# Kernel tuning notes

Hardware: AMD Instinct MI355X
Metric: run time of the kernel (lower is better)

Reference implementation:

```python
import jax, jax.numpy as jnp
import numpy as np

N_NODES = 50000
N_EDGES = 800000
IN_CH, HID_CH, OUT_CH = 128, 128, 40


def setup_inputs() -> dict:
    key = jax.random.key(0)
    k1, k2, k3, k4 = jax.random.split(key, 4)
    x = jax.random.normal(k1, (N_NODES, IN_CH), dtype=jnp.float32)
    edge_index = jax.random.randint(k2, (2, N_EDGES), 0, N_NODES, dtype=jnp.int64)
    # Glorot-ish init for linear weights
    W1 = jax.random.normal(k3, (IN_CH, HID_CH), dtype=jnp.float32) / np.sqrt(IN_CH)
    b1 = jnp.zeros((HID_CH,), dtype=jnp.float32)
    W2 = jax.random.normal(k4, (HID_CH, OUT_CH), dtype=jnp.float32) / np.sqrt(HID_CH)
    b2 = jnp.zeros((OUT_CH,), dtype=jnp.float32)
    return {"x": x, "edge_index": edge_index, "W1": W1, "b1": b1, "W2": W2, "b2": b2}


def _gcn_conv(x, src, dst, W, b):
    # GCNConv(normalize=False): dense transform then sparse aggregation (scatter-add)
    h = x @ W                                   # [N, C_out]
    out = jax.ops.segment_sum(h[src], dst, num_segments=N_NODES)  # sum_{j->i} h[j]
    return out + b


def reference(x, edge_index, W1, b1, W2, b2):
    src, dst = edge_index[0], edge_index[1]
    h = _gcn_conv(x, src, dst, W1, b1)
    h = jax.nn.relu(h)
    # dropout is identity in eval mode
    h = _gcn_conv(h, src, dst, W2, b2)
    return jax.nn.log_softmax(h, axis=-1)
```

## Files before the change

kernel.cpp:

```cpp
#include <hip/hip_runtime.h>

#define NN 50000
#define NE 800000
#define NBKT 196
#define NB_BIN 128
#define EPB (NE / NB_BIN)
#define MATN (NBKT * NB_BIN)

using short8 = __attribute__((ext_vector_type(8))) short;
using f32x4  = __attribute__((ext_vector_type(4))) float;
union U4S8 { uint4 u; short8 v; };

__device__ __forceinline__ float lof(unsigned v) { return __uint_as_float(v << 16); }
__device__ __forceinline__ float hif(unsigned v) { return __uint_as_float(v & 0xffff0000u); }
__device__ __forceinline__ unsigned bf16rne(float f) {
    unsigned u = __float_as_uint(f);
    return (u + 0x7fffu + ((u >> 16) & 1u)) >> 16;
}
__device__ __forceinline__ unsigned pack2(float a, float b) {
    return bf16rne(a) | (bf16rne(b) << 16);
}
__device__ __forceinline__ unsigned fp8pack4(float a0, float a1, float a2, float a3) {
    int w = __builtin_amdgcn_cvt_pk_fp8_f32(a0, a1, 0, false);
    w = __builtin_amdgcn_cvt_pk_fp8_f32(a2, a3, w, true);
    return (unsigned)w;
}

__global__ __launch_bounds__(256) void binhist_k(const int* __restrict__ dst,
                                                 int* __restrict__ mat,
                                                 const float* __restrict__ W1,
                                                 const float* __restrict__ W2,
                                                 unsigned* __restrict__ W1T,
                                                 unsigned* __restrict__ W2T) {
    __shared__ int hist[NBKT];
    const int tid = threadIdx.x;
    for (int i = tid; i < NBKT; i += 256) hist[i] = 0;

    const int g = blockIdx.x * 256 + tid;
    if (g < 8192) {
        const int n = g >> 6, k2 = (g & 63) * 2;
        W1T[g] = pack2(W1[k2 * 128 + n], W1[(k2 + 1) * 128 + n]);
    } else if (g < 8192 + 3072) {
        const int u = g - 8192;
        const int n = u >> 6;
        const int q0 = (u & 63) * 2, q1 = q0 + 1;
        const int c0 = (q0 & 7) * 16 + (q0 >> 3);
        const int c1 = (q1 & 7) * 16 + (q1 >> 3);
        W2T[u] = (n < 40) ? pack2(W2[c0 * 40 + n], W2[c1 * 40 + n]) : 0u;
    }
    __syncthreads();

    const int base = blockIdx.x * EPB;
    for (int e = base + tid; e < base + EPB; e += 256)
        atomicAdd(&hist[dst[e] >> 8], 1);
    __syncthreads();
    for (int i = tid; i < NBKT; i += 256)
        mat[i * NB_BIN + blockIdx.x] = hist[i];
}

__global__ __launch_bounds__(256) void binscatter_k(const int* __restrict__ src,
                                                    const int* __restrict__ dst,
                                                    const int* __restrict__ mat,
                                                    unsigned* __restrict__ binned,
                                                    int* __restrict__ bucketoff) {
    __shared__ int lds[MATN];
    __shared__ int tsum[256];
    const int tid = threadIdx.x;
    for (int i = tid; i < MATN; i += 256) lds[i] = mat[i];
    __syncthreads();
    const int b0 = tid * (MATN / 256);
    int s = 0;
#pragma unroll 7
    for (int i = 0; i < MATN / 256; ++i) s += lds[b0 + i];
    tsum[tid] = s;
    __syncthreads();
#pragma unroll
    for (int off = 1; off < 256; off <<= 1) {
        int u = (tid >= off) ? tsum[tid - off] : 0;
        __syncthreads();
        tsum[tid] += u;
        __syncthreads();
    }
    int run = tsum[tid] - s;
#pragma unroll 7
    for (int i = 0; i < MATN / 256; ++i) {
        const int v = lds[b0 + i]; lds[b0 + i] = run; run += v;
    }
    __syncthreads();

    if (blockIdx.x == 0) {
        for (int i = tid; i < NBKT; i += 256) bucketoff[i] = lds[i * NB_BIN];
        if (tid == 0) bucketoff[NBKT] = NE;
        __syncthreads();
    }

    const int base = blockIdx.x * EPB;
    for (int e = base + tid; e < base + EPB; e += 256) {
        const int d = dst[e];
        const int p = atomicAdd(&lds[(d >> 8) * NB_BIN + blockIdx.x], 1);
        binned[p] = ((unsigned)(d & 255) << 16) | (unsigned)src[e];
    }
}

__global__ __launch_bounds__(256) void bucketcsr_k(const unsigned* __restrict__ binned,
                                                   const int* __restrict__ bucketoff,
                                                   int* __restrict__ rowoff,
                                                   unsigned short* __restrict__ eid) {
    __shared__ int cnt[256];
    __shared__ int off[256];
    const int b = blockIdx.x;
    const int tid = threadIdx.x;
    const int beg = bucketoff[b];
    const int end = bucketoff[b + 1];
    cnt[tid] = 0;
    __syncthreads();
    for (int i = beg + tid; i < end; i += 256)
        atomicAdd(&cnt[(binned[i] >> 16) & 255u], 1);
    __syncthreads();
    const int v = cnt[tid];
    off[tid] = v;
    __syncthreads();
#pragma unroll
    for (int o = 1; o < 256; o <<= 1) {
        int u = (tid >= o) ? off[tid - o] : 0;
        __syncthreads();
        off[tid] += u;
        __syncthreads();
    }
    const int excl = off[tid] - v;
    const int node = b * 256 + tid;
    if (node <= NN) rowoff[node] = beg + excl;
    cnt[tid] = excl;
    __syncthreads();
    for (int i = beg + tid; i < end; i += 256) {
        const unsigned e = binned[i];
        const int p = atomicAdd(&cnt[(e >> 16) & 255u], 1);
        eid[beg + p] = (unsigned short)(e & 0xffffu);
    }
}

__global__ __launch_bounds__(256) void gemm1_k(const float* __restrict__ x,
                                               const unsigned* __restrict__ W1T,
                                               uint2* __restrict__ H1) {
    const int lane = threadIdx.x & 63;
    const int cl = lane & 15;
    const int kh = lane >> 4;
    const int gw = (blockIdx.x * 256 + threadIdx.x) >> 6;

    short8 Bf[8][4];
#pragma unroll
    for (int c = 0; c < 8; ++c)
#pragma unroll
        for (int kc = 0; kc < 4; ++kc) {
            U4S8 tb;
            tb.u = *(const uint4*)(W1T + ((c * 16 + cl) * 128 + kc * 32 + kh * 8) / 2);
            Bf[c][kc] = tb.v;
        }

    for (int mt = gw; mt < 3125; mt += 2048) {
        const int r0 = mt * 16;
        const float* ap = x + (long)(r0 + cl) * 128 + kh * 8;
        f32x4 acc[8];
#pragma unroll
        for (int c = 0; c < 8; ++c) acc[c] = (f32x4){0.f, 0.f, 0.f, 0.f};
#pragma unroll
        for (int kc = 0; kc < 4; ++kc) {
            const float4 p0 = *(const float4*)(ap + kc * 32);
            const float4 p1 = *(const float4*)(ap + kc * 32 + 4);
            U4S8 af;
            af.u.x = pack2(p0.x, p0.y);
            af.u.y = pack2(p0.z, p0.w);
            af.u.z = pack2(p1.x, p1.y);
            af.u.w = pack2(p1.z, p1.w);
#pragma unroll
            for (int c = 0; c < 8; ++c)
                acc[c] = __builtin_amdgcn_mfma_f32_16x16x32_bf16(af.v, Bf[c][kc], acc[c], 0, 0, 0);
        }
#pragma unroll
        for (int j = 0; j < 4; ++j) {
            uint2 o;
            o.x = fp8pack4(acc[0][j], acc[1][j], acc[2][j], acc[3][j]);
            o.y = fp8pack4(acc[4][j], acc[5][j], acc[6][j], acc[7][j]);
            H1[(long)(r0 + kh * 4 + j) * 16 + cl] = o;
        }
    }
}

__global__ __launch_bounds__(256) void gather1_k(const uint2* __restrict__ H1,
                                                 const int* __restrict__ rowoff,
                                                 const unsigned short* __restrict__ eid,
                                                 const float* __restrict__ b1,
                                                 uint4* __restrict__ h) {
    const int n = blockIdx.x * 4 + (threadIdx.x >> 6);
    const int lane = threadIdx.x & 63;
    const int g = lane >> 4;
    const int cl = lane & 15;
    const int beg = rowoff[n], end = rowoff[n + 1];
    float a[8] = {0.f, 0.f, 0.f, 0.f, 0.f, 0.f, 0.f, 0.f};

#define ACC8(v)                                                              \
    {                                                                        \
        auto t0 = __builtin_amdgcn_cvt_pk_f32_fp8((int)(v).x, false);        \
        auto t1 = __builtin_amdgcn_cvt_pk_f32_fp8((int)(v).x, true);         \
        auto t2 = __builtin_amdgcn_cvt_pk_f32_fp8((int)(v).y, false);        \
        auto t3 = __builtin_amdgcn_cvt_pk_f32_fp8((int)(v).y, true);         \
        a[0] += t0[0]; a[1] += t0[1]; a[2] += t1[0]; a[3] += t1[1];          \
        a[4] += t2[0]; a[5] += t2[1]; a[6] += t3[0]; a[7] += t3[1];          \
    }

    int k = beg;
    for (; k + 7 < end; k += 8) {
        const int sA = eid[k + g];
        const int sB = eid[k + 4 + g];
        const uint2 vA = H1[sA * 16 + cl];
        const uint2 vB = H1[sB * 16 + cl];
        ACC8(vA);
        ACC8(vB);
    }
    for (; k + 3 < end; k += 4) {
        const uint2 v = H1[eid[k + g] * 16 + cl];
        ACC8(v);
    }
    if (k + g < end) {
        const uint2 v = H1[eid[k + g] * 16 + cl];
        ACC8(v);
    }
#undef ACC8

#pragma unroll
    for (int i = 0; i < 8; ++i) {
        a[i] += __shfl_xor(a[i], 16, 64);
        a[i] += __shfl_xor(a[i], 32, 64);
    }
    if (lane < 16) {
        float r[8];
#pragma unroll
        for (int i = 0; i < 8; ++i) r[i] = fmaxf(a[i] + b1[i * 16 + cl], 0.f);
        uint4 o;
        o.x = pack2(r[0], r[1]);
        o.y = pack2(r[2], r[3]);
        o.z = pack2(r[4], r[5]);
        o.w = pack2(r[6], r[7]);
        h[n * 16 + cl] = o;
    }
}

__global__ __launch_bounds__(256) void gemm2_k(const unsigned* __restrict__ h,
                                               const unsigned* __restrict__ W2T,
                                               unsigned short* __restrict__ H2) {
    const int lane = threadIdx.x & 63;
    const int cl = lane & 15;
    const int kh = lane >> 4;
    const int gw = (blockIdx.x * 256 + threadIdx.x) >> 6;

    short8 Bf[3][4];
#pragma unroll
    for (int c = 0; c < 3; ++c)
#pragma unroll
        for (int kc = 0; kc < 4; ++kc) {
            U4S8 tb;
            tb.u = *(const uint4*)(W2T + ((c * 16 + cl) * 128 + kc * 32 + kh * 8) / 2);
            Bf[c][kc] = tb.v;
        }

    for (int mt = gw; mt < 3125; mt += 2048) {
        const int r0 = mt * 16;
        const unsigned* ap = h + (long)(r0 + cl) * 64 + kh * 4;
        f32x4 acc[3];
#pragma unroll
        for (int c = 0; c < 3; ++c) acc[c] = (f32x4){0.f, 0.f, 0.f, 0.f};
#pragma unroll
        for (int kc = 0; kc < 4; ++kc) {
            U4S8 af;
            af.u = *(const uint4*)(ap + kc * 16);
#pragma unroll
            for (int c = 0; c < 3; ++c)
                acc[c] = __builtin_amdgcn_mfma_f32_16x16x32_bf16(af.v, Bf[c][kc], acc[c], 0, 0, 0);
        }
        unsigned short* hp = H2 + (long)(r0 + kh * 4) * 64;
#pragma unroll
        for (int c = 0; c < 3; ++c) {
            const int col = c * 16 + cl;
            if (col < 40) {
#pragma unroll
                for (int j = 0; j < 4; ++j)
                    hp[j * 64 + col] = (unsigned short)bf16rne(acc[c][j]);
            }
        }
    }
}

__global__ __launch_bounds__(256) void gather2_k(const unsigned* __restrict__ H2,
                                                 const int* __restrict__ rowoff,
                                                 const unsigned short* __restrict__ eid,
                                                 const float* __restrict__ b2,
                                                 float* __restrict__ out) {
    const int n = blockIdx.x * 4 + (threadIdx.x >> 6);
    const int lane = threadIdx.x & 63;
    const int g = lane / 20;
    const int c2 = lane - g * 20;
    const int beg = rowoff[n], end = rowoff[n + 1];
    float ax = 0.f, ay = 0.f;
    if (g < 3) {
        int k = beg + g;
        for (; k + 3 < end; k += 6) {
            const int s0 = eid[k], s1 = eid[k + 3];
            const unsigned v0 = H2[s0 * 32 + c2];
            const unsigned v1 = H2[s1 * 32 + c2];
            ax += lof(v0) + lof(v1);
            ay += hif(v0) + hif(v1);
        }
        if (k < end) {
            const unsigned v = H2[eid[k] * 32 + c2];
            ax += lof(v); ay += hif(v);
        }
    }
    ax += __shfl(ax, lane + 20, 64) + __shfl(ax, lane + 40, 64);
    ay += __shfl(ay, lane + 20, 64) + __shfl(ay, lane + 40, 64);

    const bool act = (lane < 20);
    float2 b = {0.f, 0.f};
    if (act) b = ((const float2*)b2)[lane];
    const float vx = ax + b.x, vy = ay + b.y;
    float m = act ? fmaxf(vx, vy) : -INFINITY;
#pragma unroll
    for (int off = 32; off; off >>= 1) m = fmaxf(m, __shfl_xor(m, off, 64));
    float e = act ? (expf(vx - m) + expf(vy - m)) : 0.f;
#pragma unroll
    for (int off = 32; off; off >>= 1) e += __shfl_xor(e, off, 64);
    const float ls = logf(e);
    if (act) {
        float2 o = {vx - m - ls, vy - m - ls};
        ((float2*)out)[n * 20 + lane] = o;
    }
}

extern "C" void kernel_launch(void* const* d_in, const int* in_sizes, int n_in,
                              void* d_out, int out_size, void* d_ws, size_t ws_size,
                              hipStream_t stream) {
    const float* x  = (const float*)d_in[0];
    const int*   ei = (const int*)d_in[1];
    const float* W1 = (const float*)d_in[2];
    const float* b1 = (const float*)d_in[3];
    const float* W2 = (const float*)d_in[4];
    const float* b2 = (const float*)d_in[5];
    const int* src = ei;
    const int* dst = ei + NE;

    unsigned* H1   = (unsigned*)d_ws;
    unsigned* h    = H1 + (size_t)NN * 32;
    unsigned* H2   = h + (size_t)NN * 64;
    unsigned* W1T  = H2 + (size_t)NN * 32;
    unsigned* W2T  = W1T + 8192;
    int* mat       = (int*)(W2T + 3072);
    int* bucketoff = mat + MATN;
    int* rowoff    = bucketoff + NBKT + 1;
    unsigned short* eid = (unsigned short*)(rowoff + NN + 1);
    unsigned* binned = h;
    float* out     = (float*)d_out;

    binhist_k<<<NB_BIN, 256, 0, stream>>>(dst, mat, W1, W2, W1T, W2T);
    binscatter_k<<<NB_BIN, 256, 0, stream>>>(src, dst, mat, binned, bucketoff);
    bucketcsr_k<<<NBKT, 256, 0, stream>>>(binned, bucketoff, rowoff, eid);
    gemm1_k<<<512, 256, 0, stream>>>(x, W1T, (uint2*)H1);
    gather1_k<<<12500, 256, 0, stream>>>((const uint2*)H1, rowoff, eid, b1, (uint4*)h);
    gemm2_k<<<512, 256, 0, stream>>>(h, W2T, (unsigned short*)H2);
    gather2_k<<<12500, 256, 0, stream>>>(H2, rowoff, eid, b2, out);
}
```

Baseline: 121.9 us.

## Fuse CSR build with GEMM1, widen gather loads, shrink binning and GEMM grids

Merges the bucket-CSR kernel and the first GEMM into one launch so the two independent stages run concurrently across blocks, removing a kernel boundary. The gathers now use wider per-lane loads (uint4 fp8 rows for layer 1, uint2 bf16 for layer 2) with more edges in flight per wavefront. The binning block count and GEMM grid sizes are halved. Together these aim to cut launch overhead and raise memory-level parallelism in the gathers, at the cost of fewer lanes per row and more shuffle reduction steps.

```diff
diff --git a/kernel.cpp b/kernel.cpp
--- a/kernel.cpp
+++ b/kernel.cpp
@@ -3,9 +3,10 @@
 #define NN 50000
 #define NE 800000
 #define NBKT 196
-#define NB_BIN 128
+#define NB_BIN 64
 #define EPB (NE / NB_BIN)
 #define MATN (NBKT * NB_BIN)
+#define MCH (MATN / 256)
 
 using short8 = __attribute__((ext_vector_type(8))) short;
 using f32x4  = __attribute__((ext_vector_type(4))) float;
@@ -68,10 +69,10 @@
     const int tid = threadIdx.x;
     for (int i = tid; i < MATN; i += 256) lds[i] = mat[i];
     __syncthreads();
-    const int b0 = tid * (MATN / 256);
+    const int b0 = tid * MCH;
     int s = 0;
 #pragma unroll 7
-    for (int i = 0; i < MATN / 256; ++i) s += lds[b0 + i];
+    for (int i = 0; i < MCH; ++i) s += lds[b0 + i];
     tsum[tid] = s;
     __syncthreads();
 #pragma unroll
@@ -83,7 +84,7 @@
     }
     int run = tsum[tid] - s;
 #pragma unroll 7
-    for (int i = 0; i < MATN / 256; ++i) {
+    for (int i = 0; i < MCH; ++i) {
         const int v = lds[b0 + i]; lds[b0 + i] = run; run += v;
     }
     __syncthreads();
@@ -102,50 +103,51 @@
     }
 }
 
-__global__ __launch_bounds__(256) void bucketcsr_k(const unsigned* __restrict__ binned,
-                                                   const int* __restrict__ bucketoff,
-                                                   int* __restrict__ rowoff,
-                                                   unsigned short* __restrict__ eid) {
+__global__ __launch_bounds__(256) void csrgemm1_k(const unsigned* __restrict__ binned,
+                                                  const int* __restrict__ bucketoff,
+                                                  int* __restrict__ rowoff,
+                                                  unsigned short* __restrict__ eid,
+                                                  const float* __restrict__ x,
+                                                  const unsigned* __restrict__ W1T,
+                                                  uint2* __restrict__ H1) {
     __shared__ int cnt[256];
     __shared__ int off[256];
-    const int b = blockIdx.x;
     const int tid = threadIdx.x;
-    const int beg = bucketoff[b];
-    const int end = bucketoff[b + 1];
-    cnt[tid] = 0;
-    __syncthreads();
-    for (int i = beg + tid; i < end; i += 256)
-        atomicAdd(&cnt[(binned[i] >> 16) & 255u], 1);
-    __syncthreads();
-    const int v = cnt[tid];
-    off[tid] = v;
-    __syncthreads();
-#pragma unroll
-    for (int o = 1; o < 256; o <<= 1) {
-        int u = (tid >= o) ? off[tid - o] : 0;
-        __syncthreads();
-        off[tid] += u;
-        __syncthreads();
-    }
-    const int excl = off[tid] - v;
-    const int node = b * 256 + tid;
-    if (node <= NN) rowoff[node] = beg + excl;
-    cnt[tid] = excl;
-    __syncthreads();
-    for (int i = beg + tid; i < end; i += 256) {
-        const unsigned e = binned[i];
-        const int p = atomicAdd(&cnt[(e >> 16) & 255u], 1);
-        eid[beg + p] = (unsigned short)(e & 0xffffu);
-    }
-}
-
-__global__ __launch_bounds__(256) void gemm1_k(const float* __restrict__ x,
-                                               const unsigned* __restrict__ W1T,
-                                               uint2* __restrict__ H1) {
-    const int lane = threadIdx.x & 63;
+    if (blockIdx.x < NBKT) {
+        const int b = blockIdx.x;
+        const int beg = bucketoff[b];
+        const int end = bucketoff[b + 1];
+        cnt[tid] = 0;
+        __syncthreads();
+        for (int i = beg + tid; i < end; i += 256)
+            atomicAdd(&cnt[(binned[i] >> 16) & 255u], 1);
+        __syncthreads();
+        const int v = cnt[tid];
+        off[tid] = v;
+        __syncthreads();
+#pragma unroll
+        for (int o = 1; o < 256; o <<= 1) {
+            int u = (tid >= o) ? off[tid - o] : 0;
+            __syncthreads();
+            off[tid] += u;
+            __syncthreads();
+        }
+        const int excl = off[tid] - v;
+        const int node = b * 256 + tid;
+        if (node <= NN) rowoff[node] = beg + excl;
+        cnt[tid] = excl;
+        __syncthreads();
+        for (int i = beg + tid; i < end; i += 256) {
+            const unsigned e = binned[i];
+            const int p = atomicAdd(&cnt[(e >> 16) & 255u], 1);
+            eid[beg + p] = (unsigned short)(e & 0xffffu);
+        }
+        return;
+    }
+    const int lane = tid & 63;
     const int cl = lane & 15;
     const int kh = lane >> 4;
-    const int gw = (blockIdx.x * 256 + threadIdx.x) >> 6;
+    const int gw = ((blockIdx.x - NBKT) * 256 + tid) >> 6;
 
     short8 Bf[8][4];
 #pragma unroll
@@ -157,7 +159,7 @@
             Bf[c][kc] = tb.v;
         }
 
-    for (int mt = gw; mt < 3125; mt += 2048) {
+    for (int mt = gw; mt < 3125; mt += 1024) {
         const int r0 = mt * 16;
         const float* ap = x + (long)(r0 + cl) * 128 + kh * 8;
         f32x4 acc[8];
@@ -186,62 +188,71 @@
     }
 }
 
-__global__ __launch_bounds__(256) void gather1_k(const uint2* __restrict__ H1,
+__global__ __launch_bounds__(256) void gather1_k(const uint4* __restrict__ H1,
                                                  const int* __restrict__ rowoff,
                                                  const unsigned short* __restrict__ eid,
                                                  const float* __restrict__ b1,
                                                  uint4* __restrict__ h) {
     const int n = blockIdx.x * 4 + (threadIdx.x >> 6);
     const int lane = threadIdx.x & 63;
-    const int g = lane >> 4;
-    const int cl = lane & 15;
+    const int g = lane >> 3;
+    const int cl = lane & 7;
     const int beg = rowoff[n], end = rowoff[n + 1];
-    float a[8] = {0.f, 0.f, 0.f, 0.f, 0.f, 0.f, 0.f, 0.f};
-
-#define ACC8(v)                                                              \
+    float a[16];
+#pragma unroll
+    for (int i = 0; i < 16; ++i) a[i] = 0.f;
+
+#define ACC16(v)                                                             \
     {                                                                        \
         auto t0 = __builtin_amdgcn_cvt_pk_f32_fp8((int)(v).x, false);        \
         auto t1 = __builtin_amdgcn_cvt_pk_f32_fp8((int)(v).x, true);         \
         auto t2 = __builtin_amdgcn_cvt_pk_f32_fp8((int)(v).y, false);        \
         auto t3 = __builtin_amdgcn_cvt_pk_f32_fp8((int)(v).y, true);         \
-        a[0] += t0[0]; a[1] += t0[1]; a[2] += t1[0]; a[3] += t1[1];          \
-        a[4] += t2[0]; a[5] += t2[1]; a[6] += t3[0]; a[7] += t3[1];          \
+        auto t4 = __builtin_amdgcn_cvt_pk_f32_fp8((int)(v).z, false);        \
+        auto t5 = __builtin_amdgcn_cvt_pk_f32_fp8((int)(v).z, true);         \
+        auto t6 = __builtin_amdgcn_cvt_pk_f32_fp8((int)(v).w, false);        \
+        auto t7 = __builtin_amdgcn_cvt_pk_f32_fp8((int)(v).w, true);         \
+        a[0] += t0[0];  a[1] += t0[1];  a[2] += t1[0];  a[3] += t1[1];       \
+        a[4] += t2[0];  a[5] += t2[1];  a[6] += t3[0];  a[7] += t3[1];       \
+        a[8] += t4[0];  a[9] += t4[1];  a[10] += t5[0]; a[11] += t5[1];      \
+        a[12] += t6[0]; a[13] += t6[1]; a[14] += t7[0]; a[15] += t7[1];      \
     }
 
     int k = beg;
+    for (; k + 15 < end; k += 16) {
+        const uint4 vA = H1[eid[k + g] * 8 + cl];
+        const uint4 vB = H1[eid[k + 8 + g] * 8 + cl];
+        ACC16(vA);
+        ACC16(vB);
+    }
     for (; k + 7 < end; k += 8) {
-        const int sA = eid[k + g];
-        const int sB = eid[k + 4 + g];
-        const uint2 vA = H1[sA * 16 + cl];
-        const uint2 vB = H1[sB * 16 + cl];
-        ACC8(vA);
-        ACC8(vB);
-    }
-    for (; k + 3 < end; k += 4) {
-        const uint2 v = H1[eid[k + g] * 16 + cl];
-        ACC8(v);
+        const uint4 v = H1[eid[k + g] * 8 + cl];
+        ACC16(v);
     }
     if (k + g < end) {
-        const uint2 v = H1[eid[k + g] * 16 + cl];
-        ACC8(v);
-    }
-#undef ACC8
-
-#pragma unroll
-    for (int i = 0; i < 8; ++i) {
+        const uint4 v = H1[eid[k + g] * 8 + cl];
+        ACC16(v);
+    }
+#undef ACC16
+
+#pragma unroll
+    for (int i = 0; i < 16; ++i) {
+        a[i] += __shfl_xor(a[i], 8, 64);
         a[i] += __shfl_xor(a[i], 16, 64);
         a[i] += __shfl_xor(a[i], 32, 64);
     }
-    if (lane < 16) {
-        float r[8];
-#pragma unroll
-        for (int i = 0; i < 8; ++i) r[i] = fmaxf(a[i] + b1[i * 16 + cl], 0.f);
-        uint4 o;
-        o.x = pack2(r[0], r[1]);
-        o.y = pack2(r[2], r[3]);
-        o.z = pack2(r[4], r[5]);
-        o.w = pack2(r[6], r[7]);
-        h[n * 16 + cl] = o;
+    if (lane < 8) {
+        float r[16];
+#pragma unroll
+        for (int i = 0; i < 16; ++i)
+            r[i] = fmaxf(a[i] + b1[(i & 7) * 16 + cl * 2 + (i >> 3)], 0.f);
+        uint4 o1, o2;
+        o1.x = pack2(r[0], r[1]);  o1.y = pack2(r[2], r[3]);
+        o1.z = pack2(r[4], r[5]);  o1.w = pack2(r[6], r[7]);
+        o2.x = pack2(r[8], r[9]);  o2.y = pack2(r[10], r[11]);
+        o2.z = pack2(r[12], r[13]); o2.w = pack2(r[14], r[15]);
+        h[n * 16 + cl * 2] = o1;
+        h[n * 16 + cl * 2 + 1] = o2;
     }
 }
 
@@ -263,7 +274,7 @@
             Bf[c][kc] = tb.v;
         }
 
-    for (int mt = gw; mt < 3125; mt += 2048) {
+    for (int mt = gw; mt < 3125; mt += 1024) {
         const int r0 = mt * 16;
         const unsigned* ap = h + (long)(r0 + cl) * 64 + kh * 4;
         f32x4 acc[3];
@@ -290,48 +301,54 @@
     }
 }
 
-__global__ __launch_bounds__(256) void gather2_k(const unsigned* __restrict__ H2,
+__global__ __launch_bounds__(256) void gather2_k(const uint2* __restrict__ H2,
                                                  const int* __restrict__ rowoff,
                                                  const unsigned short* __restrict__ eid,
                                                  const float* __restrict__ b2,
                                                  float* __restrict__ out) {
     const int n = blockIdx.x * 4 + (threadIdx.x >> 6);
     const int lane = threadIdx.x & 63;
-    const int g = lane / 20;
-    const int c2 = lane - g * 20;
+    const int g = lane / 10;
+    const int c2 = lane - g * 10;
     const int beg = rowoff[n], end = rowoff[n + 1];
-    float ax = 0.f, ay = 0.f;
-    if (g < 3) {
+    float ax = 0.f, ay = 0.f, az = 0.f, aw = 0.f;
+    if (g < 6) {
         int k = beg + g;
-        for (; k + 3 < end; k += 6) {
-            const int s0 = eid[k], s1 = eid[k + 3];
-            const unsigned v0 = H2[s0 * 32 + c2];
-            const unsigned v1 = H2[s1 * 32 + c2];
-            ax += lof(v0) + lof(v1);
-            ay += hif(v0) + hif(v1);
+        for (; k + 6 < end; k += 12) {
+            const uint2 v0 = H2[eid[k] * 16 + c2];
+            const uint2 v1 = H2[eid[k + 6] * 16 + c2];
+            ax += lof(v0.x) + lof(v1.x);
+            ay += hif(v0.x) + hif(v1.x);
+            az += lof(v0.y) + lof(v1.y);
+            aw += hif(v0.y) + hif(v1.y);
         }
         if (k < end) {
-            const unsigned v = H2[eid[k] * 32 + c2];
-            ax += lof(v); ay += hif(v);
-        }
-    }
-    ax += __shfl(ax, lane + 20, 64) + __shfl(ax, lane + 40, 64);
-    ay += __shfl(ay, lane + 20, 64) + __shfl(ay, lane + 40, 64);
-
-    const bool act = (lane < 20);
-    float2 b = {0.f, 0.f};
-    if (act) b = ((const float2*)b2)[lane];
-    const float vx = ax + b.x, vy = ay + b.y;
-    float m = act ? fmaxf(vx, vy) : -INFINITY;
+            const uint2 v = H2[eid[k] * 16 + c2];
+            ax += lof(v.x); ay += hif(v.x);
+            az += lof(v.y); aw += hif(v.y);
+        }
+    }
+    ax += __shfl(ax, lane + 30, 64); ay += __shfl(ay, lane + 30, 64);
+    az += __shfl(az, lane + 30, 64); aw += __shfl(aw, lane + 30, 64);
+    ax += __shfl(ax, lane + 10, 64) + __shfl(ax, lane + 20, 64);
+    ay += __shfl(ay, lane + 10, 64) + __shfl(ay, lane + 20, 64);
+    az += __shfl(az, lane + 10, 64) + __shfl(az, lane + 20, 64);
+    aw += __shfl(aw, lane + 10, 64) + __shfl(aw, lane + 20, 64);
+
+    const bool act = (lane < 10);
+    float4 b = {0.f, 0.f, 0.f, 0.f};
+    if (act) b = ((const float4*)b2)[lane];
+    const float vx = ax + b.x, vy = ay + b.y, vz = az + b.z, vw = aw + b.w;
+    float m = act ? fmaxf(fmaxf(vx, vy), fmaxf(vz, vw)) : -INFINITY;
 #pragma unroll
     for (int off = 32; off; off >>= 1) m = fmaxf(m, __shfl_xor(m, off, 64));
-    float e = act ? (expf(vx - m) + expf(vy - m)) : 0.f;
+    float e = act ? (expf(vx - m) + expf(vy - m) + expf(vz - m) + expf(vw - m)) : 0.f;
 #pragma unroll
     for (int off = 32; off; off >>= 1) e += __shfl_xor(e, off, 64);
     const float ls = logf(e);
     if (act) {
-        float2 o = {vx - m - ls, vy - m - ls};
-        ((float2*)out)[n * 20 + lane] = o;
+        float4 o = {vx - m - ls, vy - m - ls, vz - m - ls, vw - m - ls};
+        ((float4*)(out + (long)n * 40))[lane] = o;
     }
 }
 
@@ -361,9 +378,9 @@
 
     binhist_k<<<NB_BIN, 256, 0, stream>>>(dst, mat, W1, W2, W1T, W2T);
     binscatter_k<<<NB_BIN, 256, 0, stream>>>(src, dst, mat, binned, bucketoff);
-    bucketcsr_k<<<NBKT, 256, 0, stream>>>(binned, bucketoff, rowoff, eid);
-    gemm1_k<<<512, 256, 0, stream>>>(x, W1T, (uint2*)H1);
-    gather1_k<<<12500, 256, 0, stream>>>((const uint2*)H1, rowoff, eid, b1, (uint4*)h);
-    gemm2_k<<<512, 256, 0, stream>>>(h, W2T, (unsigned short*)H2);
-    gather2_k<<<12500, 256, 0, stream>>>(H2, rowoff, eid, b2, out);
-}
+    csrgemm1_k<<<NBKT + 256, 256, 0, stream>>>(binned, bucketoff, rowoff, eid,
+                                               x, W1T, (uint2*)H1);
+    gather1_k<<<12500, 256, 0, stream>>>((const uint4*)H1, rowoff, eid, b1, (uint4*)h);
+    gemm2_k<<<256, 256, 0, stream>>>(h, W2T, (unsigned short*)H2);
+    gather2_k<<<12500, 256, 0, stream>>>((const uint2*)H2, rowoff, eid, b2, out);
+}
```

Measured after the change: 132.4 us. +8.6%, slower.
